# Kernel optimization log

Measured on AMD Instinct MI355X. Metric: run time of the kernel, lower is better.

Reference implementation:

```python
import jax, jax.numpy as jnp
import numpy as np

N_NODES = 50000
SEQ_LEN = 32
N_TOKENS = 100000
EMB_DIM = 128          # in_feats / 2
IN_FEATS = 256
N_HIDDEN = 256
N_CLASSES = 40
N_EDGES = 800000
PAD_IX = 0


def setup_inputs() -> dict:
    key = jax.random.key(0)
    k1, k2, k3, k4, k5, k6 = jax.random.split(key, 6)
    features = jax.random.randint(k1, (N_NODES, SEQ_LEN), 0, N_TOKENS, dtype=jnp.int32)
    src = jax.random.randint(k2, (N_EDGES,), 0, N_NODES, dtype=jnp.int32)
    dst = jax.random.randint(k3, (N_EDGES,), 0, N_NODES, dtype=jnp.int32)
    emb_table = jax.random.normal(k4, (N_TOKENS, EMB_DIM), dtype=jnp.float32) * 0.02
    W1 = jax.random.normal(k5, (IN_FEATS, N_HIDDEN), dtype=jnp.float32) * 0.02
    b1 = jnp.zeros((N_HIDDEN,), dtype=jnp.float32)
    W2 = jax.random.normal(k6, (N_HIDDEN, N_CLASSES), dtype=jnp.float32) * 0.02
    b2 = jnp.zeros((N_CLASSES,), dtype=jnp.float32)
    return {"features": features, "src": src, "dst": dst,
            "emb_table": emb_table, "W1": W1, "b1": b1, "W2": W2, "b2": b2}


def _apply_embs(features, emb_table):
    # padding_idx row contributes zeros (nn.Embedding padding_idx semantics)
    emb = emb_table.at[PAD_IX].set(0.0)
    h = emb[features]                                    # [N, L, D]
    seq_len = jnp.sum(features != PAD_IX, axis=1)        # [N]
    seq_len = jnp.maximum(seq_len, 1)[:, None].astype(h.dtype)
    h1 = h.sum(axis=1) / seq_len                         # masked mean
    h2 = h.max(axis=1)                                   # max pool (pads are 0)
    return jnp.concatenate((h1, h2), axis=1)             # [N, 2D]


def _graph_conv(h, src, dst, norm_s, norm_d, W, b):
    # DGL GraphConv, norm='both': out = D_in^{-1/2} A D_out^{-1/2} h W + b
    hw = h @ W                                           # transform first (smaller msgs)
    m = (hw * norm_s[:, None])[src]                      # gather messages [E, F]
    agg = jax.ops.segment_sum(m, dst, num_segments=N_NODES)
    return agg * norm_d[:, None] + b


def reference(features, src, dst, emb_table, W1, b1, W2, b2):
    ones_e = jnp.ones((src.shape[0],), dtype=jnp.float32)
    deg_out = jnp.maximum(jax.ops.segment_sum(ones_e, src, num_segments=N_NODES), 1.0)
    deg_in = jnp.maximum(jax.ops.segment_sum(ones_e, dst, num_segments=N_NODES), 1.0)
    norm_s = deg_out ** -0.5
    norm_d = deg_in ** -0.5

    h = _apply_embs(features, emb_table)                 # [N, in_feats]
    h = jax.nn.relu(_graph_conv(h, src, dst, norm_s, norm_d, W1, b1))
    # dropout is identity in eval mode
    h = _graph_conv(h, src, dst, norm_s, norm_d, W2, b2)
    return h                                             # [N, n_classes]
```

## Files before the change

kernel.cpp:

```cpp
#include <hip/hip_runtime.h>
#include <math.h>

#define N_NODES 50000
#define SEQ_LEN 32
#define EMB_DIM 128
#define IN_FEATS 256
#define N_HIDDEN 256
#define N_CLASSES 40
#define N_EDGES 800000
#define N_TOKENS 100000

#define SLOT 64
#define NBIN 196
#define BINCAP 4608
#define EPB 4000

typedef short short8 __attribute__((ext_vector_type(8)));
typedef float f32x4 __attribute__((ext_vector_type(4)));

__device__ __forceinline__ unsigned short f2bf(float x) {
  unsigned int u = __float_as_uint(x);
  unsigned int r = (u + 0x7FFFu + ((u >> 16) & 1u)) >> 16;
  return (unsigned short)r;
}
__device__ __forceinline__ float bf2f(unsigned short s) {
  return __uint_as_float((unsigned int)s << 16);
}
__device__ __forceinline__ unsigned int pack2bf(float a, float b) {
  return (unsigned int)f2bf(a) | ((unsigned int)f2bf(b) << 16);
}

__global__ __launch_bounds__(256) void k_binA(const int* __restrict__ src,
                                              const int* __restrict__ dst,
                                              int* __restrict__ gcntD,
                                              int* __restrict__ gcntS,
                                              unsigned int* __restrict__ dbin,
                                              unsigned char* __restrict__ sbin) {
  __shared__ int cntD[NBIN], cntS[NBIN], baseD[NBIN], baseS[NBIN];
  int tid = threadIdx.x;
  if (tid < NBIN) { cntD[tid] = 0; cntS[tid] = 0; }
  __syncthreads();
  int e0 = blockIdx.x * EPB;
  for (int j = tid; j < EPB; j += 256) {
    int d = dst[e0 + j], s = src[e0 + j];
    atomicAdd(&cntD[d >> 8], 1);
    atomicAdd(&cntS[s >> 8], 1);
  }
  __syncthreads();
  if (tid < NBIN) {
    baseD[tid] = atomicAdd(&gcntD[tid], cntD[tid]);
    baseS[tid] = atomicAdd(&gcntS[tid], cntS[tid]);
    cntD[tid] = 0;
    cntS[tid] = 0;
  }
  __syncthreads();
  for (int j = tid; j < EPB; j += 256) {
    int d = dst[e0 + j], s = src[e0 + j];
    int bd = d >> 8, bs = s >> 8;
    int od = atomicAdd(&cntD[bd], 1);
    int pd = baseD[bd] + od;
    if (pd < BINCAP) dbin[(size_t)bd * BINCAP + pd] = ((unsigned int)s << 8) | (unsigned int)(d & 255);
    int os = atomicAdd(&cntS[bs], 1);
    int ps = baseS[bs] + os;
    if (ps < BINCAP) sbin[(size_t)bs * BINCAP + ps] = (unsigned char)(s & 255);
  }
}

__global__ __launch_bounds__(256) void k_binB(const unsigned int* __restrict__ dbin,
                                              const int* __restrict__ gcntD,
                                              int* __restrict__ cursor,
                                              int* __restrict__ csr_pad) {
  __shared__ int cnt[256];
  int tid = threadIdx.x, b = blockIdx.x;
  cnt[tid] = 0;
  __syncthreads();
  int n = min(gcntD[b], BINCAP);
  const unsigned int* bb = dbin + (size_t)b * BINCAP;
  for (int j = tid; j < n; j += 256) {
    unsigned int e = bb[j];
    int lo = e & 255;
    int slot = atomicAdd(&cnt[lo], 1);
    if (slot < SLOT) csr_pad[(size_t)(b * 256 + lo) * SLOT + slot] = (int)(e >> 8);
  }
  __syncthreads();
  int node = b * 256 + tid;
  if (node < N_NODES) cursor[node] = min(cnt[tid], SLOT);
}

__global__ __launch_bounds__(256) void k_degout(const unsigned char* __restrict__ sbin,
                                                const int* __restrict__ gcntS,
                                                int* __restrict__ deg_out) {
  __shared__ int cnt[256];
  int tid = threadIdx.x, b = blockIdx.x;
  cnt[tid] = 0;
  __syncthreads();
  int n = min(gcntS[b], BINCAP);
  const unsigned char* bb = sbin + (size_t)b * BINCAP;
  for (int j = tid; j < n; j += 256) atomicAdd(&cnt[bb[j]], 1);
  __syncthreads();
  int node = b * 256 + tid;
  if (node < N_NODES) deg_out[node] = cnt[tid];
}

__global__ __launch_bounds__(256) void k_norm(const int* __restrict__ deg_out,
                                              const int* __restrict__ cursor,
                                              float* __restrict__ norm_s,
                                              float* __restrict__ norm_d) {
  int i = blockIdx.x * 256 + threadIdx.x;
  if (i < N_NODES) {
    norm_s[i] = 1.0f / sqrtf((float)max(deg_out[i], 1));
    norm_d[i] = 1.0f / sqrtf((float)max(cursor[i], 1));
  }
}

__global__ __launch_bounds__(256) void k_emb2bf(const float* __restrict__ emb,
                                                unsigned short* __restrict__ emb_b) {
  const int total = N_TOKENS * EMB_DIM / 4;
  for (int i = blockIdx.x * 256 + threadIdx.x; i < total; i += gridDim.x * 256) {
    float4 v = ((const float4*)emb)[i];
    ushort4 o;
    o.x = f2bf(v.x); o.y = f2bf(v.y); o.z = f2bf(v.z); o.w = f2bf(v.w);
    ((ushort4*)emb_b)[i] = o;
  }
}

__global__ __launch_bounds__(256) void k_packW1(const float* __restrict__ W,
                                                unsigned short* __restrict__ Wp) {
  int g = blockIdx.x * 256 + threadIdx.x;
  int lane = g & 63, jb = (g >> 6) & 15, kt = g >> 10;
  int col = jb * 16 + (lane & 15);
  int kbase = kt * 32 + (lane >> 4) * 8;
  unsigned short* o = Wp + (size_t)g * 8;
  #pragma unroll
  for (int e = 0; e < 8; ++e) o[e] = f2bf(W[(size_t)(kbase + e) * N_HIDDEN + col]);
}

__global__ __launch_bounds__(256) void k_packW2(const float* __restrict__ W,
                                                unsigned short* __restrict__ Wp) {
  int g = blockIdx.x * 256 + threadIdx.x;
  if (g >= 8 * 3 * 64) return;
  int lane = g & 63, jb = (g >> 6) % 3, kt = g / (3 * 64);
  int col = jb * 16 + (lane & 15);
  int kbase = kt * 32 + (lane >> 4) * 8;
  unsigned short* o = Wp + (size_t)g * 8;
  #pragma unroll
  for (int e = 0; e < 8; ++e)
    o[e] = (col < N_CLASSES) ? f2bf(W[(size_t)(kbase + e) * N_CLASSES + col]) : (unsigned short)0;
}

__global__ __launch_bounds__(256) void k_embed(const int* __restrict__ feats,
                                               const uint2* __restrict__ rows2,
                                               uint2* __restrict__ h) {
  int tid = threadIdx.x;
  int w = tid >> 6, lane = tid & 63;
  int node = blockIdx.x * 4 + w;
  int laneL = lane & 31, half = lane >> 5;

  int tok0 = feats[(size_t)node * SEQ_LEN + laneL];
  unsigned long long m = __ballot(laneL < 32 && tok0 != 0);
  int cnt = (int)__popcll(m & 0xFFFFFFFFull);
  float inv = 1.0f / (float)max(cnt, 1);

  float s0 = 0.f, s1 = 0.f, s2 = 0.f, s3 = 0.f;
  float m0 = -INFINITY, m1 = -INFINITY, m2 = -INFINITY, m3 = -INFINITY;
  #pragma unroll
  for (int t = 0; t < 16; ++t) {
    int tok = __shfl(tok0, 2 * t + half);
    uint2 v = make_uint2(0u, 0u);
    if (tok) v = rows2[(size_t)tok * 32 + laneL];
    float f0 = bf2f((unsigned short)(v.x & 0xFFFF));
    float f1 = bf2f((unsigned short)(v.x >> 16));
    float f2 = bf2f((unsigned short)(v.y & 0xFFFF));
    float f3 = bf2f((unsigned short)(v.y >> 16));
    s0 += f0; s1 += f1; s2 += f2; s3 += f3;
    m0 = fmaxf(m0, f0); m1 = fmaxf(m1, f1);
    m2 = fmaxf(m2, f2); m3 = fmaxf(m3, f3);
  }
  s0 += __shfl_xor(s0, 32); s1 += __shfl_xor(s1, 32);
  s2 += __shfl_xor(s2, 32); s3 += __shfl_xor(s3, 32);
  m0 = fmaxf(m0, __shfl_xor(m0, 32)); m1 = fmaxf(m1, __shfl_xor(m1, 32));
  m2 = fmaxf(m2, __shfl_xor(m2, 32)); m3 = fmaxf(m3, __shfl_xor(m3, 32));

  if (half == 0) {
    uint2* hv = h + (size_t)node * 64;
    hv[laneL]      = make_uint2(pack2bf(s0 * inv, s1 * inv), pack2bf(s2 * inv, s3 * inv));
    hv[32 + laneL] = make_uint2(pack2bf(m0, m1), pack2bf(m2, m3));
  }
}

__global__ __launch_bounds__(256) void k_mm1(const unsigned short* __restrict__ hb,
                                             const unsigned short* __restrict__ Wp,
                                             const float* __restrict__ norm_s,
                                             unsigned short* __restrict__ out) {
  __shared__ unsigned short sA[64 * 256];
  int tid = threadIdx.x;
  int r0 = blockIdx.x * 64;
  #pragma unroll
  for (int it = 0; it < 8; ++it) {
    int idx = it * 256 + tid;
    int r = idx >> 5, kb = idx & 31;
    uint4 v = make_uint4(0, 0, 0, 0);
    int row = r0 + r;
    if (row < N_NODES) v = *(const uint4*)(hb + (size_t)row * 256 + kb * 8);
    *(uint4*)&sA[r * 256 + ((kb ^ (r & 7)) << 3)] = v;
  }
  __syncthreads();

  int w = tid >> 6, lane = tid & 63;
  const short8* W8 = (const short8*)Wp;
  f32x4 acc[4][4];
  #pragma unroll
  for (int i = 0; i < 4; ++i)
    #pragma unroll
    for (int j = 0; j < 4; ++j) acc[i][j] = (f32x4){0.f, 0.f, 0.f, 0.f};

  #pragma unroll
  for (int kt = 0; kt < 8; ++kt) {
    short8 a[4], b[4];
    int kb = kt * 4 + (lane >> 4);
    #pragma unroll
    for (int ri = 0; ri < 4; ++ri) {
      int r = ri * 16 + (lane & 15);
      a[ri] = *(const short8*)&sA[r * 256 + ((kb ^ (r & 7)) << 3)];
    }
    #pragma unroll
    for (int jb = 0; jb < 4; ++jb) b[jb] = W8[(kt * 16 + w * 4 + jb) * 64 + lane];
    #pragma unroll
    for (int ri = 0; ri < 4; ++ri)
      #pragma unroll
      for (int jb = 0; jb < 4; ++jb)
        acc[ri][jb] = __builtin_amdgcn_mfma_f32_16x16x32_bf16(a[ri], b[jb], acc[ri][jb], 0, 0, 0);
  }

  #pragma unroll
  for (int ri = 0; ri < 4; ++ri) {
    #pragma unroll
    for (int rr = 0; rr < 4; ++rr) {
      int row = r0 + ri * 16 + (lane >> 4) * 4 + rr;
      if (row < N_NODES) {
        float ns = norm_s[row];
        #pragma unroll
        for (int jb = 0; jb < 4; ++jb) {
          int col = w * 64 + jb * 16 + (lane & 15);
          out[(size_t)row * 256 + col] = f2bf(acc[ri][jb][rr] * ns);
        }
      }
    }
  }
}

__global__ __launch_bounds__(256) void k_agg1(const uint2* __restrict__ rows2,
                                              const int* __restrict__ cursor,
                                              const int* __restrict__ csr_pad,
                                              const float* __restrict__ norm_d,
                                              const float* __restrict__ b1,
                                              uint2* __restrict__ out) {
  int tid = threadIdx.x;
  int w = tid >> 6, lane = tid & 63;
  int node = blockIdx.x * 4 + w;
  int cnt = __builtin_amdgcn_readfirstlane(cursor[node]);
  const int* csr = csr_pad + (size_t)node * SLOT;

  float a0 = 0.f, a1 = 0.f, a2 = 0.f, a3 = 0.f;
  int e = 0;
  for (; e + 8 <= cnt; e += 8) {
    int s[8];
    #pragma unroll
    for (int i = 0; i < 8; ++i) s[i] = csr[e + i];
    #pragma unroll
    for (int i = 0; i < 8; ++i) {
      uint2 v = rows2[(size_t)s[i] * 64 + lane];
      a0 += bf2f((unsigned short)(v.x & 0xFFFF));
      a1 += bf2f((unsigned short)(v.x >> 16));
      a2 += bf2f((unsigned short)(v.y & 0xFFFF));
      a3 += bf2f((unsigned short)(v.y >> 16));
    }
  }
  for (; e + 4 <= cnt; e += 4) {
    int s[4];
    #pragma unroll
    for (int i = 0; i < 4; ++i) s[i] = csr[e + i];
    #pragma unroll
    for (int i = 0; i < 4; ++i) {
      uint2 v = rows2[(size_t)s[i] * 64 + lane];
      a0 += bf2f((unsigned short)(v.x & 0xFFFF));
      a1 += bf2f((unsigned short)(v.x >> 16));
      a2 += bf2f((unsigned short)(v.y & 0xFFFF));
      a3 += bf2f((unsigned short)(v.y >> 16));
    }
  }
  for (; e < cnt; ++e) {
    uint2 v = rows2[(size_t)csr[e] * 64 + lane];
    a0 += bf2f((unsigned short)(v.x & 0xFFFF));
    a1 += bf2f((unsigned short)(v.x >> 16));
    a2 += bf2f((unsigned short)(v.y & 0xFFFF));
    a3 += bf2f((unsigned short)(v.y >> 16));
  }

  float nd = norm_d[node];
  float4 bb = *(const float4*)&b1[4 * lane];
  float o0 = fmaxf(a0 * nd + bb.x, 0.f);
  float o1 = fmaxf(a1 * nd + bb.y, 0.f);
  float o2 = fmaxf(a2 * nd + bb.z, 0.f);
  float o3 = fmaxf(a3 * nd + bb.w, 0.f);
  out[(size_t)node * 64 + lane] = make_uint2(pack2bf(o0, o1), pack2bf(o2, o3));
}

__global__ __launch_bounds__(256) void k_mm2(const unsigned short* __restrict__ h2b,
                                             const unsigned short* __restrict__ Wp,
                                             const float* __restrict__ norm_s,
                                             unsigned short* __restrict__ out) {
  __shared__ unsigned short sA[64 * 256];
  int tid = threadIdx.x;
  int r0 = blockIdx.x * 64;
  #pragma unroll
  for (int it = 0; it < 8; ++it) {
    int idx = it * 256 + tid;
    int r = idx >> 5, kb = idx & 31;
    uint4 v = make_uint4(0, 0, 0, 0);
    int row = r0 + r;
    if (row < N_NODES) v = *(const uint4*)(h2b + (size_t)row * 256 + kb * 8);
    *(uint4*)&sA[r * 256 + ((kb ^ (r & 7)) << 3)] = v;
  }
  __syncthreads();

  int w = tid >> 6, lane = tid & 63;
  const short8* W8 = (const short8*)Wp;
  f32x4 acc[3];
  #pragma unroll
  for (int j = 0; j < 3; ++j) acc[j] = (f32x4){0.f, 0.f, 0.f, 0.f};

  #pragma unroll
  for (int kt = 0; kt < 8; ++kt) {
    int r = w * 16 + (lane & 15);
    int kb = kt * 4 + (lane >> 4);
    short8 a = *(const short8*)&sA[r * 256 + ((kb ^ (r & 7)) << 3)];
    #pragma unroll
    for (int jb = 0; jb < 3; ++jb) {
      short8 b = W8[(kt * 3 + jb) * 64 + lane];
      acc[jb] = __builtin_amdgcn_mfma_f32_16x16x32_bf16(a, b, acc[jb], 0, 0, 0);
    }
  }

  #pragma unroll
  for (int rr = 0; rr < 4; ++rr) {
    int row = r0 + w * 16 + (lane >> 4) * 4 + rr;
    if (row < N_NODES) {
      float ns = norm_s[row];
      #pragma unroll
      for (int jb = 0; jb < 3; ++jb) {
        int col = jb * 16 + (lane & 15);
        if (col < N_CLASSES) out[(size_t)row * N_CLASSES + col] = f2bf(acc[jb][rr] * ns);
      }
    }
  }
}

__global__ __launch_bounds__(256) void k_agg2(const unsigned int* __restrict__ rows,
                                              const int* __restrict__ cursor,
                                              const int* __restrict__ csr_pad,
                                              const float* __restrict__ norm_d,
                                              const float* __restrict__ b2,
                                              float* __restrict__ out) {
  int tid = threadIdx.x;
  int w = tid >> 6, lane = tid & 63;
  int node = blockIdx.x * 4 + w;
  int slot = lane / 20, fl = lane % 20;
  int cnt = __builtin_amdgcn_readfirstlane(cursor[node]);
  const int* csr = csr_pad + (size_t)node * SLOT;

  float a0 = 0.f, a1 = 0.f;
  if (slot < 3) {
    for (int e = slot; e < cnt; e += 3) {
      int s = csr[e];
      unsigned int v = rows[(size_t)s * 20 + fl];
      a0 += bf2f((unsigned short)(v & 0xFFFF));
      a1 += bf2f((unsigned short)(v >> 16));
    }
  }
  float p0 = __shfl(a0, lane + 20), p1 = __shfl(a1, lane + 20);
  float q0 = __shfl(a0, lane + 40), q1 = __shfl(a1, lane + 40);
  if (slot == 0) {
    a0 += p0 + q0; a1 += p1 + q1;
    float nd = norm_d[node];
    float o0 = a0 * nd + b2[2 * fl];
    float o1 = a1 * nd + b2[2 * fl + 1];
    *(float2*)&out[(size_t)node * N_CLASSES + 2 * fl] = make_float2(o0, o1);
  }
}

extern "C" void kernel_launch(void* const* d_in, const int* in_sizes, int n_in,
                              void* d_out, int out_size, void* d_ws, size_t ws_size,
                              hipStream_t stream) {
  const int*   feats = (const int*)d_in[0];
  const int*   src   = (const int*)d_in[1];
  const int*   dst   = (const int*)d_in[2];
  const float* emb   = (const float*)d_in[3];
  const float* W1    = (const float*)d_in[4];
  const float* b1    = (const float*)d_in[5];
  const float* W2    = (const float*)d_in[6];
  const float* b2    = (const float*)d_in[7];
  float* out = (float*)d_out;

  char* base = (char*)d_ws;
  size_t off = 0;
  auto alloc = [&](size_t bytes) -> char* {
    char* p = base + off;
    off += (bytes + 255) & ~(size_t)255;
    return p;
  };
  unsigned short* hb      = (unsigned short*)alloc((size_t)N_NODES * IN_FEATS * 2);
  unsigned short* msgb    = (unsigned short*)alloc((size_t)N_NODES * N_HIDDEN * 2);
  unsigned short* hw2b    = (unsigned short*)alloc((size_t)N_NODES * N_CLASSES * 2);
  unsigned short* emb_b   = (unsigned short*)alloc((size_t)N_TOKENS * EMB_DIM * 2);
  unsigned short* Wp1     = (unsigned short*)alloc((size_t)8 * 16 * 64 * 8 * 2);
  unsigned short* Wp2     = (unsigned short*)alloc((size_t)8 * 3 * 64 * 8 * 2);
  int*   gcnt    = (int*)alloc((size_t)512 * 4);
  int*   gcntD   = gcnt;
  int*   gcntS   = gcnt + 256;
  int*   cursor  = (int*)alloc((size_t)N_NODES * 4);
  int*   deg_out = (int*)alloc((size_t)N_NODES * 4);
  float* norm_s  = (float*)alloc((size_t)N_NODES * 4);
  float* norm_d  = (float*)alloc((size_t)N_NODES * 4);
  unsigned int*  dbin = (unsigned int*)alloc((size_t)NBIN * BINCAP * 4);
  unsigned char* sbin = (unsigned char*)alloc((size_t)NBIN * BINCAP);
  int*   csr_pad = (int*)alloc((size_t)N_NODES * SLOT * 4);

  hipMemsetAsync(gcnt, 0, 512 * 4, stream);

  int nb = (N_NODES + 255) / 256;
  k_emb2bf<<<2048, 256, 0, stream>>>(emb, emb_b);
  k_packW1<<<32, 256, 0, stream>>>(W1, Wp1);
  k_packW2<<<6, 256, 0, stream>>>(W2, Wp2);
  k_binA<<<N_EDGES / EPB, 256, 0, stream>>>(src, dst, gcntD, gcntS, dbin, sbin);
  k_binB<<<NBIN, 256, 0, stream>>>(dbin, gcntD, cursor, csr_pad);
  k_degout<<<NBIN, 256, 0, stream>>>(sbin, gcntS, deg_out);
  k_norm<<<nb, 256, 0, stream>>>(deg_out, cursor, norm_s, norm_d);

  int gemm_blocks = (N_NODES + 63) / 64;
  k_embed<<<N_NODES / 4, 256, 0, stream>>>(feats, (const uint2*)emb_b, (uint2*)hb);
  k_mm1<<<gemm_blocks, 256, 0, stream>>>(hb, Wp1, norm_s, msgb);
  k_agg1<<<N_NODES / 4, 256, 0, stream>>>((const uint2*)msgb, cursor, csr_pad, norm_d, b1, (uint2*)hb);
  k_mm2<<<gemm_blocks, 256, 0, stream>>>(hb, Wp2, norm_s, hw2b);
  k_agg2<<<N_NODES / 4, 256, 0, stream>>>((const unsigned int*)hw2b, cursor, csr_pad, norm_d, b2, out);
}
```

Baseline: 230.3 us.

## Merge prep and norm kernels, widen embed and agg1 gathers to 16-byte loads

Three small prep kernels (embedding bf16 conversion and two weight packs) become one launch, and the out-degree count now computes both norms directly, dropping the separate norm kernel and the deg_out buffer. The embedding pooling and layer-1 aggregation kernels switch from 8-byte to 16-byte per-lane loads. Each wavefront therefore gathers several rows at once and reduces across lane groups with shuffles. This cuts launch count and load-instruction count, at the cost of extra cross-lane reductions and more registers per thread.

```diff
diff --git a/kernel.cpp b/kernel.cpp
--- a/kernel.cpp
+++ b/kernel.cpp
@@ -28,6 +28,43 @@
 }
 __device__ __forceinline__ unsigned int pack2bf(float a, float b) {
   return (unsigned int)f2bf(a) | ((unsigned int)f2bf(b) << 16);
+}
+
+__global__ __launch_bounds__(256) void k_prep(const float* __restrict__ emb,
+                                              unsigned short* __restrict__ emb_b,
+                                              const float* __restrict__ W1,
+                                              unsigned short* __restrict__ Wp1,
+                                              const float* __restrict__ W2,
+                                              unsigned short* __restrict__ Wp2) {
+  int b = blockIdx.x, tid = threadIdx.x;
+  if (b < 2048) {
+    const int total = N_TOKENS * EMB_DIM / 4;
+    for (int i = b * 256 + tid; i < total; i += 2048 * 256) {
+      float4 v = ((const float4*)emb)[i];
+      ushort4 o;
+      o.x = f2bf(v.x); o.y = f2bf(v.y); o.z = f2bf(v.z); o.w = f2bf(v.w);
+      ((ushort4*)emb_b)[i] = o;
+    }
+  } else if (b < 2080) {
+    int g = (b - 2048) * 256 + tid;
+    int lane = g & 63, jb = (g >> 6) & 15, kt = g >> 10;
+    int col = jb * 16 + (lane & 15);
+    int kbase = kt * 32 + (lane >> 4) * 8;
+    unsigned short* o = Wp1 + (size_t)g * 8;
+    #pragma unroll
+    for (int e = 0; e < 8; ++e) o[e] = f2bf(W1[(size_t)(kbase + e) * N_HIDDEN + col]);
+  } else {
+    int g = (b - 2080) * 256 + tid;
+    if (g < 8 * 3 * 64) {
+      int lane = g & 63, jb = (g >> 6) % 3, kt = g / (3 * 64);
+      int col = jb * 16 + (lane & 15);
+      int kbase = kt * 32 + (lane >> 4) * 8;
+      unsigned short* o = Wp2 + (size_t)g * 8;
+      #pragma unroll
+      for (int e = 0; e < 8; ++e)
+        o[e] = (col < N_CLASSES) ? f2bf(W2[(size_t)(kbase + e) * N_CLASSES + col]) : (unsigned short)0;
+    }
+  }
 }
 
 __global__ __launch_bounds__(256) void k_binA(const int* __restrict__ src,
@@ -87,9 +124,11 @@
   if (node < N_NODES) cursor[node] = min(cnt[tid], SLOT);
 }
 
-__global__ __launch_bounds__(256) void k_degout(const unsigned char* __restrict__ sbin,
-                                                const int* __restrict__ gcntS,
-                                                int* __restrict__ deg_out) {
+__global__ __launch_bounds__(256) void k_degoutnorm(const unsigned char* __restrict__ sbin,
+                                                    const int* __restrict__ gcntS,
+                                                    const int* __restrict__ cursor,
+                                                    float* __restrict__ norm_s,
+                                                    float* __restrict__ norm_d) {
   __shared__ int cnt[256];
   int tid = threadIdx.x, b = blockIdx.x;
   cnt[tid] = 0;
@@ -99,92 +138,59 @@
   for (int j = tid; j < n; j += 256) atomicAdd(&cnt[bb[j]], 1);
   __syncthreads();
   int node = b * 256 + tid;
-  if (node < N_NODES) deg_out[node] = cnt[tid];
-}
-
-__global__ __launch_bounds__(256) void k_norm(const int* __restrict__ deg_out,
-                                              const int* __restrict__ cursor,
-                                              float* __restrict__ norm_s,
-                                              float* __restrict__ norm_d) {
-  int i = blockIdx.x * 256 + threadIdx.x;
-  if (i < N_NODES) {
-    norm_s[i] = 1.0f / sqrtf((float)max(deg_out[i], 1));
-    norm_d[i] = 1.0f / sqrtf((float)max(cursor[i], 1));
-  }
-}
-
-__global__ __launch_bounds__(256) void k_emb2bf(const float* __restrict__ emb,
-                                                unsigned short* __restrict__ emb_b) {
-  const int total = N_TOKENS * EMB_DIM / 4;
-  for (int i = blockIdx.x * 256 + threadIdx.x; i < total; i += gridDim.x * 256) {
-    float4 v = ((const float4*)emb)[i];
-    ushort4 o;
-    o.x = f2bf(v.x); o.y = f2bf(v.y); o.z = f2bf(v.z); o.w = f2bf(v.w);
-    ((ushort4*)emb_b)[i] = o;
-  }
-}
-
-__global__ __launch_bounds__(256) void k_packW1(const float* __restrict__ W,
-                                                unsigned short* __restrict__ Wp) {
-  int g = blockIdx.x * 256 + threadIdx.x;
-  int lane = g & 63, jb = (g >> 6) & 15, kt = g >> 10;
-  int col = jb * 16 + (lane & 15);
-  int kbase = kt * 32 + (lane >> 4) * 8;
-  unsigned short* o = Wp + (size_t)g * 8;
-  #pragma unroll
-  for (int e = 0; e < 8; ++e) o[e] = f2bf(W[(size_t)(kbase + e) * N_HIDDEN + col]);
-}
-
-__global__ __launch_bounds__(256) void k_packW2(const float* __restrict__ W,
-                                                unsigned short* __restrict__ Wp) {
-  int g = blockIdx.x * 256 + threadIdx.x;
-  if (g >= 8 * 3 * 64) return;
-  int lane = g & 63, jb = (g >> 6) % 3, kt = g / (3 * 64);
-  int col = jb * 16 + (lane & 15);
-  int kbase = kt * 32 + (lane >> 4) * 8;
-  unsigned short* o = Wp + (size_t)g * 8;
-  #pragma unroll
-  for (int e = 0; e < 8; ++e)
-    o[e] = (col < N_CLASSES) ? f2bf(W[(size_t)(kbase + e) * N_CLASSES + col]) : (unsigned short)0;
+  if (node < N_NODES) {
+    norm_s[node] = 1.0f / sqrtf((float)max(cnt[tid], 1));
+    norm_d[node] = 1.0f / sqrtf((float)max(cursor[node], 1));
+  }
 }
 
 __global__ __launch_bounds__(256) void k_embed(const int* __restrict__ feats,
-                                               const uint2* __restrict__ rows2,
-                                               uint2* __restrict__ h) {
+                                               const uint4* __restrict__ rows4,
+                                               uint4* __restrict__ h4) {
   int tid = threadIdx.x;
   int w = tid >> 6, lane = tid & 63;
   int node = blockIdx.x * 4 + w;
-  int laneL = lane & 31, half = lane >> 5;
+  int lq = lane & 15, qg = lane >> 4;
+  int laneL = lane & 31;
 
   int tok0 = feats[(size_t)node * SEQ_LEN + laneL];
-  unsigned long long m = __ballot(laneL < 32 && tok0 != 0);
+  unsigned long long m = __ballot(tok0 != 0);
   int cnt = (int)__popcll(m & 0xFFFFFFFFull);
   float inv = 1.0f / (float)max(cnt, 1);
 
-  float s0 = 0.f, s1 = 0.f, s2 = 0.f, s3 = 0.f;
+  float s0 = 0.f, s1 = 0.f, s2 = 0.f, s3 = 0.f, s4 = 0.f, s5 = 0.f, s6 = 0.f, s7 = 0.f;
   float m0 = -INFINITY, m1 = -INFINITY, m2 = -INFINITY, m3 = -INFINITY;
-  #pragma unroll
-  for (int t = 0; t < 16; ++t) {
-    int tok = __shfl(tok0, 2 * t + half);
-    uint2 v = make_uint2(0u, 0u);
-    if (tok) v = rows2[(size_t)tok * 32 + laneL];
-    float f0 = bf2f((unsigned short)(v.x & 0xFFFF));
-    float f1 = bf2f((unsigned short)(v.x >> 16));
-    float f2 = bf2f((unsigned short)(v.y & 0xFFFF));
-    float f3 = bf2f((unsigned short)(v.y >> 16));
-    s0 += f0; s1 += f1; s2 += f2; s3 += f3;
-    m0 = fmaxf(m0, f0); m1 = fmaxf(m1, f1);
-    m2 = fmaxf(m2, f2); m3 = fmaxf(m3, f3);
-  }
-  s0 += __shfl_xor(s0, 32); s1 += __shfl_xor(s1, 32);
-  s2 += __shfl_xor(s2, 32); s3 += __shfl_xor(s3, 32);
-  m0 = fmaxf(m0, __shfl_xor(m0, 32)); m1 = fmaxf(m1, __shfl_xor(m1, 32));
-  m2 = fmaxf(m2, __shfl_xor(m2, 32)); m3 = fmaxf(m3, __shfl_xor(m3, 32));
-
-  if (half == 0) {
-    uint2* hv = h + (size_t)node * 64;
-    hv[laneL]      = make_uint2(pack2bf(s0 * inv, s1 * inv), pack2bf(s2 * inv, s3 * inv));
-    hv[32 + laneL] = make_uint2(pack2bf(m0, m1), pack2bf(m2, m3));
+  float m4 = -INFINITY, m5 = -INFINITY, m6 = -INFINITY, m7 = -INFINITY;
+  #pragma unroll
+  for (int t = 0; t < 8; ++t) {
+    int tok = __shfl(tok0, t * 4 + qg);
+    uint4 v = make_uint4(0u, 0u, 0u, 0u);
+    if (tok) v = rows4[(size_t)tok * 16 + lq];
+    float f0 = bf2f((unsigned short)(v.x & 0xFFFF)), f1 = bf2f((unsigned short)(v.x >> 16));
+    float f2 = bf2f((unsigned short)(v.y & 0xFFFF)), f3 = bf2f((unsigned short)(v.y >> 16));
+    float f4 = bf2f((unsigned short)(v.z & 0xFFFF)), f5 = bf2f((unsigned short)(v.z >> 16));
+    float f6 = bf2f((unsigned short)(v.w & 0xFFFF)), f7 = bf2f((unsigned short)(v.w >> 16));
+    s0 += f0; s1 += f1; s2 += f2; s3 += f3; s4 += f4; s5 += f5; s6 += f6; s7 += f7;
+    m0 = fmaxf(m0, f0); m1 = fmaxf(m1, f1); m2 = fmaxf(m2, f2); m3 = fmaxf(m3, f3);
+    m4 = fmaxf(m4, f4); m5 = fmaxf(m5, f5); m6 = fmaxf(m6, f6); m7 = fmaxf(m7, f7);
+  }
+  #pragma unroll
+  for (int mask = 16; mask <= 32; mask <<= 1) {
+    s0 += __shfl_xor(s0, mask); s1 += __shfl_xor(s1, mask);
+    s2 += __shfl_xor(s2, mask); s3 += __shfl_xor(s3, mask);
+    s4 += __shfl_xor(s4, mask); s5 += __shfl_xor(s5, mask);
+    s6 += __shfl_xor(s6, mask); s7 += __shfl_xor(s7, mask);
+    m0 = fmaxf(m0, __shfl_xor(m0, mask)); m1 = fmaxf(m1, __shfl_xor(m1, mask));
+    m2 = fmaxf(m2, __shfl_xor(m2, mask)); m3 = fmaxf(m3, __shfl_xor(m3, mask));
+    m4 = fmaxf(m4, __shfl_xor(m4, mask)); m5 = fmaxf(m5, __shfl_xor(m5, mask));
+    m6 = fmaxf(m6, __shfl_xor(m6, mask)); m7 = fmaxf(m7, __shfl_xor(m7, mask));
+  }
+  if (qg == 0) {
+    uint4* hv = h4 + (size_t)node * 32;
+    hv[lq] = make_uint4(pack2bf(s0 * inv, s1 * inv), pack2bf(s2 * inv, s3 * inv),
+                        pack2bf(s4 * inv, s5 * inv), pack2bf(s6 * inv, s7 * inv));
+    hv[16 + lq] = make_uint4(pack2bf(m0, m1), pack2bf(m2, m3),
+                             pack2bf(m4, m5), pack2bf(m6, m7));
   }
 }
 
@@ -249,61 +255,69 @@
   }
 }
 
-__global__ __launch_bounds__(256) void k_agg1(const uint2* __restrict__ rows2,
+__global__ __launch_bounds__(256) void k_agg1(const uint4* __restrict__ rows4,
                                               const int* __restrict__ cursor,
                                               const int* __restrict__ csr_pad,
                                               const float* __restrict__ norm_d,
                                               const float* __restrict__ b1,
-                                              uint2* __restrict__ out) {
+                                              uint4* __restrict__ out4) {
   int tid = threadIdx.x;
   int w = tid >> 6, lane = tid & 63;
   int node = blockIdx.x * 4 + w;
   int cnt = __builtin_amdgcn_readfirstlane(cursor[node]);
   const int* csr = csr_pad + (size_t)node * SLOT;
-
-  float a0 = 0.f, a1 = 0.f, a2 = 0.f, a3 = 0.f;
+  int half = lane >> 5, lq = lane & 31;
+
+  float a0 = 0.f, a1 = 0.f, a2 = 0.f, a3 = 0.f, a4 = 0.f, a5 = 0.f, a6 = 0.f, a7 = 0.f;
   int e = 0;
   for (; e + 8 <= cnt; e += 8) {
-    int s[8];
-    #pragma unroll
-    for (int i = 0; i < 8; ++i) s[i] = csr[e + i];
-    #pragma unroll
-    for (int i = 0; i < 8; ++i) {
-      uint2 v = rows2[(size_t)s[i] * 64 + lane];
-      a0 += bf2f((unsigned short)(v.x & 0xFFFF));
-      a1 += bf2f((unsigned short)(v.x >> 16));
-      a2 += bf2f((unsigned short)(v.y & 0xFFFF));
-      a3 += bf2f((unsigned short)(v.y >> 16));
-    }
-  }
-  for (; e + 4 <= cnt; e += 4) {
-    int s[4];
-    #pragma unroll
-    for (int i = 0; i < 4; ++i) s[i] = csr[e + i];
+    int s0 = csr[e + 0 + half], s1 = csr[e + 2 + half];
+    int s2 = csr[e + 4 + half], s3 = csr[e + 6 + half];
+    uint4 v0 = rows4[(size_t)s0 * 32 + lq];
+    uint4 v1 = rows4[(size_t)s1 * 32 + lq];
+    uint4 v2 = rows4[(size_t)s2 * 32 + lq];
+    uint4 v3 = rows4[(size_t)s3 * 32 + lq];
     #pragma unroll
     for (int i = 0; i < 4; ++i) {
-      uint2 v = rows2[(size_t)s[i] * 64 + lane];
-      a0 += bf2f((unsigned short)(v.x & 0xFFFF));
-      a1 += bf2f((unsigned short)(v.x >> 16));
-      a2 += bf2f((unsigned short)(v.y & 0xFFFF));
-      a3 += bf2f((unsigned short)(v.y >> 16));
-    }
-  }
-  for (; e < cnt; ++e) {
-    uint2 v = rows2[(size_t)csr[e] * 64 + lane];
-    a0 += bf2f((unsigned short)(v.x & 0xFFFF));
-    a1 += bf2f((unsigned short)(v.x >> 16));
-    a2 += bf2f((unsigned short)(v.y & 0xFFFF));
-    a3 += bf2f((unsigned short)(v.y >> 16));
-  }
-
-  float nd = norm_d[node];
-  float4 bb = *(const float4*)&b1[4 * lane];
-  float o0 = fmaxf(a0 * nd + bb.x, 0.f);
-  float o1 = fmaxf(a1 * nd + bb.y, 0.f);
-  float o2 = fmaxf(a2 * nd + bb.z, 0.f);
-  float o3 = fmaxf(a3 * nd + bb.w, 0.f);
-  out[(size_t)node * 64 + lane] = make_uint2(pack2bf(o0, o1), pack2bf(o2, o3));
+      uint4 v = (i == 0) ? v0 : (i == 1) ? v1 : (i == 2) ? v2 : v3;
+      a0 += bf2f((unsigned short)(v.x & 0xFFFF)); a1 += bf2f((unsigned short)(v.x >> 16));
+      a2 += bf2f((unsigned short)(v.y & 0xFFFF)); a3 += bf2f((unsigned short)(v.y >> 16));
+      a4 += bf2f((unsigned short)(v.z & 0xFFFF)); a5 += bf2f((unsigned short)(v.z >> 16));
+      a6 += bf2f((unsigned short)(v.w & 0xFFFF)); a7 += bf2f((unsigned short)(v.w >> 16));
+    }
+  }
+  for (; e + 2 <= cnt; e += 2) {
+    int s = csr[e + half];
+    uint4 v = rows4[(size_t)s * 32 + lq];
+    a0 += bf2f((unsigned short)(v.x & 0xFFFF)); a1 += bf2f((unsigned short)(v.x >> 16));
+    a2 += bf2f((unsigned short)(v.y & 0xFFFF)); a3 += bf2f((unsigned short)(v.y >> 16));
+    a4 += bf2f((unsigned short)(v.z & 0xFFFF)); a5 += bf2f((unsigned short)(v.z >> 16));
+    a6 += bf2f((unsigned short)(v.w & 0xFFFF)); a7 += bf2f((unsigned short)(v.w >> 16));
+  }
+  if (e < cnt) {
+    uint4 v = make_uint4(0u, 0u, 0u, 0u);
+    if (half == 0) v = rows4[(size_t)csr[e] * 32 + lq];
+    a0 += bf2f((unsigned short)(v.x & 0xFFFF)); a1 += bf2f((unsigned short)(v.x >> 16));
+    a2 += bf2f((unsigned short)(v.y & 0xFFFF)); a3 += bf2f((unsigned short)(v.y >> 16));
+    a4 += bf2f((unsigned short)(v.z & 0xFFFF)); a5 += bf2f((unsigned short)(v.z >> 16));
+    a6 += bf2f((unsigned short)(v.w & 0xFFFF)); a7 += bf2f((unsigned short)(v.w >> 16));
+  }
+  a0 += __shfl_xor(a0, 32); a1 += __shfl_xor(a1, 32);
+  a2 += __shfl_xor(a2, 32); a3 += __shfl_xor(a3, 32);
+  a4 += __shfl_xor(a4, 32); a5 += __shfl_xor(a5, 32);
+  a6 += __shfl_xor(a6, 32); a7 += __shfl_xor(a7, 32);
+
+  if (half == 0) {
+    float nd = norm_d[node];
+    float4 bb0 = *(const float4*)&b1[8 * lq];
+    float4 bb1 = *(const float4*)&b1[8 * lq + 4];
+    float o0 = fmaxf(a0 * nd + bb0.x, 0.f), o1 = fmaxf(a1 * nd + bb0.y, 0.f);
+    float o2 = fmaxf(a2 * nd + bb0.z, 0.f), o3 = fmaxf(a3 * nd + bb0.w, 0.f);
+    float o4 = fmaxf(a4 * nd + bb1.x, 0.f), o5 = fmaxf(a5 * nd + bb1.y, 0.f);
+    float o6 = fmaxf(a6 * nd + bb1.z, 0.f), o7 = fmaxf(a7 * nd + bb1.w, 0.f);
+    out4[(size_t)node * 32 + lq] = make_uint4(pack2bf(o0, o1), pack2bf(o2, o3),
+                                              pack2bf(o4, o5), pack2bf(o6, o7));
+  }
 }
 
 __global__ __launch_bounds__(256) void k_mm2(const unsigned short* __restrict__ h2b,
@@ -419,7 +433,6 @@
   int*   gcntD   = gcnt;
   int*   gcntS   = gcnt + 256;
   int*   cursor  = (int*)alloc((size_t)N_NODES * 4);
-  int*   deg_out = (int*)alloc((size_t)N_NODES * 4);
   float* norm_s  = (float*)alloc((size_t)N_NODES * 4);
   float* norm_d  = (float*)alloc((size_t)N_NODES * 4);
   unsigned int*  dbin = (unsigned int*)alloc((size_t)NBIN * BINCAP * 4);
@@ -428,19 +441,15 @@
 
   hipMemsetAsync(gcnt, 0, 512 * 4, stream);
 
-  int nb = (N_NODES + 255) / 256;
-  k_emb2bf<<<2048, 256, 0, stream>>>(emb, emb_b);
-  k_packW1<<<32, 256, 0, stream>>>(W1, Wp1);
-  k_packW2<<<6, 256, 0, stream>>>(W2, Wp2);
+  k_prep<<<2086, 256, 0, stream>>>(emb, emb_b, W1, Wp1, W2, Wp2);
   k_binA<<<N_EDGES / EPB, 256, 0, stream>>>(src, dst, gcntD, gcntS, dbin, sbin);
   k_binB<<<NBIN, 256, 0, stream>>>(dbin, gcntD, cursor, csr_pad);
-  k_degout<<<NBIN, 256, 0, stream>>>(sbin, gcntS, deg_out);
-  k_norm<<<nb, 256, 0, stream>>>(deg_out, cursor, norm_s, norm_d);
+  k_degoutnorm<<<NBIN, 256, 0, stream>>>(sbin, gcntS, cursor, norm_s, norm_d);
 
   int gemm_blocks = (N_NODES + 63) / 64;
-  k_embed<<<N_NODES / 4, 256, 0, stream>>>(feats, (const uint2*)emb_b, (uint2*)hb);
+  k_embed<<<N_NODES / 4, 256, 0, stream>>>(feats, (const uint4*)emb_b, (uint4*)hb);
   k_mm1<<<gemm_blocks, 256, 0, stream>>>(hb, Wp1, norm_s, msgb);
-  k_agg1<<<N_NODES / 4, 256, 0, stream>>>((const uint2*)msgb, cursor, csr_pad, norm_d, b1, (uint2*)hb);
+  k_agg1<<<N_NODES / 4, 256, 0, stream>>>((const uint4*)msgb, cursor, csr_pad, norm_d, b1, (uint4*)hb);
   k_mm2<<<gemm_blocks, 256, 0, stream>>>(hb, Wp2, norm_s, hw2b);
   k_agg2<<<N_NODES / 4, 256, 0, stream>>>((const unsigned int*)hw2b, cursor, csr_pad, norm_d, b2, out);
 }
```

Result: no change. 225.8 us (-1.9%).
